# Kernel optimization log

Hardware: AMD Instinct MI355X
Metric: run time of the kernel (lower is better)

## Reference

```python
import jax, jax.numpy as jnp
import numpy as np

B, S, T, E, H, Vt, Vs, M = 16, 64, 64, 256, 512, 32000, 32000, 100
J = 2 * M + 1


def _lstm(x, lengths, Wx, Wh, b, reverse=False):
    # TF LSTMCell (forget_bias=1.0) with sequence_length masking, optional reverse_sequence.
    Bn, Tn, _ = x.shape
    Hn = Wh.shape[0]
    tpos = jnp.arange(Tn)
    ridx = None
    if reverse:
        ridx = jnp.where(tpos[None, :] < lengths[:, None], lengths[:, None] - 1 - tpos[None, :], tpos[None, :])
        x = jnp.take_along_axis(x, ridx[:, :, None], axis=1)
    mask = (tpos[:, None] < lengths[None, :])[:, :, None]  # [T,B,1]
    xT = jnp.swapaxes(x, 0, 1)  # [T,B,E]

    def step(carry, inp):
        h, c = carry
        xt, mt = inp
        g = xt @ Wx + h @ Wh + b
        i, j, f, o = jnp.split(g, 4, axis=-1)
        c_new = jax.nn.sigmoid(f + 1.0) * c + jax.nn.sigmoid(i) * jnp.tanh(j)
        h_new = jax.nn.sigmoid(o) * jnp.tanh(c_new)
        c2 = jnp.where(mt, c_new, c)
        h2 = jnp.where(mt, h_new, h)
        return (h2, c2), jnp.where(mt, h_new, jnp.zeros_like(h_new))

    init = (jnp.zeros((Bn, Hn), x.dtype), jnp.zeros((Bn, Hn), x.dtype))
    _, ys = jax.lax.scan(step, init, (xT, mask))
    ys = jnp.swapaxes(ys, 0, 1)  # [B,T,H]
    if reverse:
        ys = jnp.take_along_axis(ys, ridx[:, :, None], axis=1)
    return ys


def setup_inputs() -> dict:
    key = jax.random.key(0)
    ks = jax.random.split(key, 24)
    sc = 0.05
    n = lambda k, shape: (jax.random.normal(k, shape, jnp.float32) * sc)
    inp = {
        "sources": jax.random.randint(ks[0], (B, S), 0, Vs, jnp.int32),
        "targets": jax.random.randint(ks[1], (B, T), 0, Vt, jnp.int32),
        "targets_null": jnp.array([Vt - 1], jnp.int32),
        "target_lengths": jax.random.randint(ks[2], (B,), T // 2, T + 1, jnp.int32),
        "emb": n(ks[3], (Vt, E)),
        "nnW": n(ks[4], (E, H)),
        "nnb": jnp.zeros((H,), jnp.float32),
        "Wx_fw": n(ks[5], (E, 4 * H)),
        "Wh_fw": n(ks[6], (H, 4 * H)),
        "b_fw": jnp.zeros((4 * H,), jnp.float32),
        "Wx_bw": n(ks[7], (E, 4 * H)),
        "Wh_bw": n(ks[8], (H, 4 * H)),
        "b_bw": jnp.zeros((4 * H,), jnp.float32),
        "Wproj_e": n(ks[9], (2 * H, H)),
        "Wv": n(ks[10], (H, Vs)),
        "bv": jnp.zeros((Vs,), jnp.float32),
        "Wproj_t": n(ks[11], (2 * H, E)),
        "Wj": n(ks[12], (H, J)),
        "bj": jnp.zeros((J,), jnp.float32),
        "Wp0": n(ks[13], (H, 1)),
        "bp0": jnp.zeros((1,), jnp.float32),
    }
    return inp


def reference(sources, targets, targets_null, target_lengths, emb, nnW, nnb,
              Wx_fw, Wh_fw, b_fw, Wx_bw, Wh_bw, b_bw, Wproj_e, Wv, bv,
              Wproj_t, Wj, bj, Wp0, bp0):
    x = emb[targets]                              # [B,T,E]
    x_null = emb[targets_null]                    # [1,E]
    null_state = jnp.tanh(x_null @ nnW + nnb)     # [1,H]
    h_fw = _lstm(x, target_lengths, Wx_fw, Wh_fw, b_fw, False)
    h_bw = _lstm(x, target_lengths, Wx_bw, Wh_bw, b_bw, True)
    h_cat = jnp.concatenate([h_fw, h_bw], axis=-1)  # [B,T,2H]

    # ---- emission ----
    ts = h_cat @ Wproj_e                          # [B,T,H]
    probs = jax.nn.softmax(ts @ Wv + bv, axis=-1)             # [B,T,Vs]
    null_probs = jax.nn.softmax(null_state @ Wv + bv, axis=-1)  # [1,Vs]
    e_word = jnp.take_along_axis(probs, sources[:, None, :].astype(jnp.int32), axis=2)  # [B,T,S]
    e_null = jnp.broadcast_to(null_probs[0][sources][:, None, :], e_word.shape)
    emission = jnp.concatenate([e_word, e_null], axis=1)       # [B,2T,S]

    # ---- transition ----
    tt = jnp.tanh((h_cat @ Wproj_t) @ nnW + nnb)  # [B,T,H]
    jump = jax.nn.softmax(tt @ Wj + bj, axis=-1)  # [B,T,J]
    p0 = jax.nn.sigmoid(tt @ Wp0 + bp0)[..., 0]   # [B,T]
    Tn = targets.shape[1]
    # entry (i,j) <- jump[i, M + j - i] (the tf.map_fn gather over word_idx)
    idx = M + jnp.arange(Tn)[None, :] - jnp.arange(Tn)[:, None]  # [T,T]
    jw = jnp.take_along_axis(jump, jnp.broadcast_to(idx[None], (jump.shape[0], Tn, Tn)), axis=2)  # [B,T,T]
    eye = jnp.eye(Tn, dtype=jw.dtype)
    half = jnp.concatenate([jw, p0[:, :, None] * eye], axis=2)            # [B,T,2T]
    transition = jnp.concatenate([half, half], axis=1)                    # [B,2T,2T]
    lhalf = jnp.concatenate([jnp.log(jw), jnp.log(p0)[:, :, None] * eye], axis=2)
    transition_log = jnp.concatenate([lhalf, lhalf], axis=1)
    return emission, transition, transition_log
```

## Files before the change

kernel.cpp:

```cpp
#include <hip/hip_runtime.h>
#include <hip/hip_bf16.h>
#include <math.h>

#define Bn 16
#define Sn 64
#define Tn 64
#define En 256
#define Hn 512
#define VS 32000
#define Jn 201
#define Mn 100

#define O_HCATF  0
#define O_DENOM  524288
#define O_NULLD  525312
#define O_SLOTS  525376
#define O_HBUF   527424
#define ZERO_N   560192
#define O_NS     560192
#define O_TS     560704
#define O_TSF    1084992
#define O_TTPRE  1347136
#define O_TTPF   1609280
#define O_TT     1740352
#define O_XF     2264640
#define O_WXFW   2395712
#define O_WXBW   2657856
#define O_WPEF   2920000
#define O_WPTF   3182144
#define O_NNWF   3313216
#define O_GX     3378752
#define O_WVB    2264640

typedef __attribute__((ext_vector_type(8))) short short8;
typedef __attribute__((ext_vector_type(4))) float f32x4;

__device__ __forceinline__ float sigf(float x) { return 1.0f / (1.0f + expf(-x)); }
__device__ __forceinline__ unsigned short tobf(float x) {
    __hip_bfloat16 h = __float2bfloat16(x);
    return *reinterpret_cast<unsigned short*>(&h);
}

__device__ __forceinline__ void dconvA(const float* __restrict__ A, uint4* __restrict__ out,
                                       int K, const int* __restrict__ gidx, int g) {
    int Kd = K >> 5;
    int lane = g & 63, t = g >> 6;
    int ks = t % Kd, mt = t / Kd;
    int m = mt * 16 + (lane & 15);
    int k0 = ks * 32 + (lane >> 4) * 8;
    const float* p = (gidx ? A + (size_t)gidx[m] * K : A + (size_t)m * K) + k0;
    float4 f0 = *(const float4*)(p);
    float4 f1 = *(const float4*)(p + 4);
    unsigned short u[8] = {tobf(f0.x), tobf(f0.y), tobf(f0.z), tobf(f0.w),
                           tobf(f1.x), tobf(f1.y), tobf(f1.z), tobf(f1.w)};
    out[g] = *(uint4*)u;
}

__device__ __forceinline__ void dconvB(const float* __restrict__ B, uint4* __restrict__ out,
                                       int N, int K, int g) {
    int Kd = K >> 5;
    int lane = g & 63, t = g >> 6;
    int ks = t % Kd, nt = t / Kd;
    int n = nt * 16 + (lane & 15);
    int k0 = ks * 32 + (lane >> 4) * 8;
    const float* p = B + (size_t)k0 * N + n;
    unsigned short u[8];
#pragma unroll
    for (int j = 0; j < 8; j++) u[j] = tobf(p[(size_t)j * N]);
    out[g] = *(uint4*)u;
}

__global__ __launch_bounds__(256) void convA_k(const float* __restrict__ A,
                                               uint4* __restrict__ out, int K,
                                               const int* __restrict__ gidx) {
    dconvA(A, out, K, gidx, blockIdx.x * 256 + threadIdx.x);
}
__global__ __launch_bounds__(256) void convB_k(const float* __restrict__ B,
                                               uint4* __restrict__ out, int N, int K) {
    dconvB(B, out, N, K, blockIdx.x * 256 + threadIdx.x);
}

__global__ __launch_bounds__(256) void mega_prep_k(float4* __restrict__ zdst, int zn4,
                                                   const float* __restrict__ emb,
                                                   const int* __restrict__ targets,
                                                   uint4* __restrict__ xf,
                                                   const float* __restrict__ wxfw, uint4* __restrict__ wxfwf,
                                                   const float* __restrict__ wxbw, uint4* __restrict__ wxbwf,
                                                   const float* __restrict__ wpe, uint4* __restrict__ wpef,
                                                   const float* __restrict__ wpt, uint4* __restrict__ wptf,
                                                   const float* __restrict__ nnw, uint4* __restrict__ nnwf) {
    int blk = blockIdx.x, tid = threadIdx.x;
    if (blk < 548) {
        int i = blk * 256 + tid;
        if (i < zn4) zdst[i] = make_float4(0.f, 0.f, 0.f, 0.f);
    } else if (blk < 676) {
        dconvA(emb, xf, 256, targets, (blk - 548) * 256 + tid);
    } else if (blk < 932) {
        dconvB(wxfw, wxfwf, 2048, 256, (blk - 676) * 256 + tid);
    } else if (blk < 1188) {
        dconvB(wxbw, wxbwf, 2048, 256, (blk - 932) * 256 + tid);
    } else if (blk < 1444) {
        dconvB(wpe, wpef, 512, 1024, (blk - 1188) * 256 + tid);
    } else if (blk < 1572) {
        dconvB(wpt, wptf, 256, 1024, (blk - 1444) * 256 + tid);
    } else {
        dconvB(nnw, nnwf, 512, 256, (blk - 1572) * 256 + tid);
    }
}

template <int ACT>
__global__ __launch_bounds__(256) void gemm_mfma_k(const uint4* __restrict__ af,
                                                   const uint4* __restrict__ bf,
                                                   const float* __restrict__ bias,
                                                   float* __restrict__ C, int N, int Kd) {
    int tid = threadIdx.x, w = tid >> 6, lane = tid & 63;
    int ntb = blockIdx.x * 8 + w * 2;
    int mtb = blockIdx.y * 8;
    f32x4 acc[8][2];
#pragma unroll
    for (int i = 0; i < 8; i++)
#pragma unroll
        for (int j = 0; j < 2; j++) acc[i][j] = 0.0f;
    for (int ks = 0; ks < Kd; ++ks) {
        uint4 b0 = bf[(size_t)(ntb * Kd + ks) * 64 + lane];
        uint4 b1 = bf[(size_t)((ntb + 1) * Kd + ks) * 64 + lane];
#pragma unroll
        for (int i = 0; i < 8; i++) {
            uint4 a = af[(size_t)((mtb + i) * Kd + ks) * 64 + lane];
            acc[i][0] = __builtin_amdgcn_mfma_f32_16x16x32_bf16(
                *reinterpret_cast<short8*>(&a), *reinterpret_cast<short8*>(&b0), acc[i][0], 0, 0, 0);
            acc[i][1] = __builtin_amdgcn_mfma_f32_16x16x32_bf16(
                *reinterpret_cast<short8*>(&a), *reinterpret_cast<short8*>(&b1), acc[i][1], 0, 0, 0);
        }
    }
    int n0 = ntb * 16 + (lane & 15);
    int q = lane >> 4;
    float bs0 = bias ? bias[n0] : 0.f;
    float bs1 = bias ? bias[n0 + 16] : 0.f;
#pragma unroll
    for (int i = 0; i < 8; i++)
#pragma unroll
        for (int r = 0; r < 4; r++) {
            int m = (mtb + i) * 16 + q * 4 + r;
            float v0 = acc[i][0][r] + bs0;
            float v1 = acc[i][1][r] + bs1;
            if (ACT == 1) { v0 = tanhf(v0); v1 = tanhf(v1); }
            C[(size_t)m * N + n0] = v0;
            C[(size_t)m * N + n0 + 16] = v1;
        }
}

__global__ __launch_bounds__(256) void null_fused_k(const float* __restrict__ emb,
                                                    const int* __restrict__ tnull,
                                                    const float* __restrict__ nnW,
                                                    const float* __restrict__ nnb,
                                                    const float* __restrict__ Wv,
                                                    const float* __restrict__ bv,
                                                    float* __restrict__ ns,
                                                    float* __restrict__ nd) {
    __shared__ float xn[En];
    __shared__ float nsl[Hn];
    __shared__ float red[4];
    int t = threadIdx.x;
    xn[t] = emb[(size_t)tnull[0] * En + t];
    __syncthreads();
#pragma unroll
    for (int hh = 0; hh < 2; hh++) {
        int h = t + hh * 256;
        float a = nnb[h];
        for (int e = 0; e < En; e++) a += xn[e] * nnW[(size_t)e * Hn + h];
        float v = tanhf(a);
        nsl[h] = v;
        if (blockIdx.x == 0) ns[h] = v;
    }
    __syncthreads();
    int v = blockIdx.x * 256 + t;
    float a = bv[v];
    for (int k = 0; k < Hn; k++) a += nsl[k] * Wv[(size_t)k * VS + v];
    float e = expf(a);
    for (int o = 1; o < 64; o <<= 1) e += __shfl_xor(e, o);
    if ((t & 63) == 0) red[t >> 6] = e;
    __syncthreads();
    if (t == 0) atomicAdd(nd, red[0] + red[1] + red[2] + red[3]);
}

__global__ __launch_bounds__(256, 1) void lstm_persist_k(const float* __restrict__ wh_fw,
                                                         const float* __restrict__ wh_bw,
                                                         const float* __restrict__ gx,
                                                         const int* __restrict__ lengths,
                                                         unsigned* __restrict__ hbuf32,
                                                         unsigned* __restrict__ hcat32,
                                                         unsigned* __restrict__ slots) {
    __shared__ uint4 whf[8192];
    __shared__ float raw[32][129];
    __shared__ int lenS[16];
    int tid = threadIdx.x;
    int blk = blockIdx.x;
    int dir = blk >> 4;
    int u0 = (blk & 15) * 32;
    const float* wh = dir ? wh_bw : wh_fw;
    if (tid < 16) lenS[tid] = lengths[tid];

    for (int chunk = 0; chunk < 16; ++chunk) {
#pragma unroll
        for (int it = 0; it < 16; ++it) {
            int li = it * 256 + tid;
            int kl = li >> 7, c = li & 127;
            int g = c >> 5, ub = c & 31;
            raw[kl][c] = wh[(size_t)(chunk * 32 + kl) * 2048 + g * 512 + u0 + ub];
        }
        __syncthreads();
#pragma unroll
        for (int it = 0; it < 2; ++it) {
            int idx = tid * 2 + it;
            int w = idx >> 7, t = (idx >> 6) & 1, lane = idx & 63;
            int n = lane & 15, uu = n >> 1, p = n & 1;
            int cc = (t * 2 + p) * 32 + w * 8 + uu;
            int kb = (lane >> 4) * 8;
            unsigned short u8[8];
#pragma unroll
            for (int j = 0; j < 8; j++) u8[j] = tobf(raw[kb + j][cc]);
            whf[((w * 2 + t) * 16 + chunk) * 64 + lane] = *(uint4*)u8;
        }
        __syncthreads();
    }

    int wv = tid >> 6, lane = tid & 63;
    int n = lane & 15, uu = n >> 1, q = lane >> 4;
    int u = u0 + wv * 8 + uu;
    float creg[4] = {0.f, 0.f, 0.f, 0.f};
    unsigned short hbf[4] = {0, 0, 0, 0};

    for (int s = 0; s < 64; ++s) {
        float gxi[4], gxj[4], gxf[4], gxo[4];
#pragma unroll
        for (int r = 0; r < 4; r++) {
            int b = q * 4 + r;
            int len = lenS[b];
            int tc = dir ? (len - 1 - s) : s;
            tc = tc < 0 ? 0 : tc;
            const float* gp = gx + (size_t)dir * 2097152 + (size_t)(b * 64 + tc) * 2048 + u;
            gxi[r] = gp[0]; gxj[r] = gp[512]; gxf[r] = gp[1024]; gxo[r] = gp[1536];
        }
        const unsigned long long* hb64 =
            (const unsigned long long*)(hbuf32 + (((s & 1) * 2 + dir) * 16) * 256);
        unsigned long long h64[32];
#pragma unroll
        for (int ks = 0; ks < 16; ks++) {
            int idx = n * 128 + ks * 8 + q * 2;
            h64[2 * ks] = __hip_atomic_load(hb64 + idx, __ATOMIC_RELAXED, __HIP_MEMORY_SCOPE_AGENT);
            h64[2 * ks + 1] = __hip_atomic_load(hb64 + idx + 1, __ATOMIC_RELAXED, __HIP_MEMORY_SCOPE_AGENT);
        }
        f32x4 acc0 = {0.f, 0.f, 0.f, 0.f}, acc1 = {0.f, 0.f, 0.f, 0.f};
#pragma unroll
        for (int ks = 0; ks < 16; ks++) {
            unsigned long long av[2] = {h64[2 * ks], h64[2 * ks + 1]};
            short8 a = *reinterpret_cast<short8*>(av);
            uint4 b0 = whf[((wv * 2 + 0) * 16 + ks) * 64 + lane];
            uint4 b1 = whf[((wv * 2 + 1) * 16 + ks) * 64 + lane];
            acc0 = __builtin_amdgcn_mfma_f32_16x16x32_bf16(a, *reinterpret_cast<short8*>(&b0), acc0, 0, 0, 0);
            acc1 = __builtin_amdgcn_mfma_f32_16x16x32_bf16(a, *reinterpret_cast<short8*>(&b1), acc1, 0, 0, 0);
        }
#pragma unroll
        for (int r = 0; r < 4; r++) {
            float jvv = __shfl_xor(acc0[r], 1);
            float ovv = __shfl_xor(acc1[r], 1);
            int b = q * 4 + r;
            int len = lenS[b];
            float gi = acc0[r] + gxi[r];
            float gj = jvv + gxj[r];
            float gf = acc1[r] + gxf[r];
            float go = ovv + gxo[r];
            float cn = sigf(gf + 1.0f) * creg[r] + sigf(gi) * tanhf(gj);
            float hn = sigf(go) * tanhf(cn);
            if (s < len) { creg[r] = cn; hbf[r] = tobf(hn); }
        }
#pragma unroll
        for (int r = 0; r < 4; r++) {
            unsigned self = hbf[r];
            unsigned part = (unsigned)__shfl_xor((int)self, 2) & 0xffffu;
            if ((n & 3) == 0) {
                unsigned pk = self | (part << 16);
                int b = q * 4 + r;
                __hip_atomic_store(
                    hbuf32 + ((((s + 1) & 1) * 2 + dir) * 16 + b) * 256 + (u >> 1), pk,
                    __ATOMIC_RELAXED, __HIP_MEMORY_SCOPE_AGENT);
                int len = lenS[b];
                if (s < len) {
                    int tin = dir ? (len - 1 - s) : s;
                    int row = b * 64 + tin, col = dir * 512 + u;
                    int mt = row >> 4, ksx = col >> 5;
                    int lanep = (row & 15) | (((col >> 3) & 3) << 4);
                    hcat32[(size_t)(((mt * 32 + ksx) * 64 + lanep) * 4) + ((col & 7) >> 1)] = pk;
                }
            }
        }
        if (s == 63) break;
        __syncthreads();
        if (tid == 0)
            __hip_atomic_store(&slots[blk * 64], (unsigned)(s + 1), __ATOMIC_RELAXED,
                               __HIP_MEMORY_SCOPE_AGENT);
        if (tid < 16) {
            while (__hip_atomic_load(&slots[(dir * 16 + tid) * 64], __ATOMIC_RELAXED,
                                     __HIP_MEMORY_SCOPE_AGENT) < (unsigned)(s + 1)) {
                __builtin_amdgcn_s_sleep(1);
            }
        }
        __syncthreads();
    }
}

__global__ __launch_bounds__(256) void phaseA_mfma_k(const uint4* __restrict__ tsb,
                                                     const uint4* __restrict__ wvb,
                                                     const float* __restrict__ bv,
                                                     float* __restrict__ denom) {
    __shared__ float redL[4][128];
    int tid = threadIdx.x;
    int wave = tid >> 6, lane = tid & 63;
    int ntbase = blockIdx.x * 8 + wave * 2;
    float bv0 = bv[ntbase * 16 + (lane & 15)];
    float bv1 = bv[(ntbase + 1) * 16 + (lane & 15)];
    int q = lane >> 4;
    for (int mc = 0; mc < 8; ++mc) {
        f32x4 acc[8][2];
#pragma unroll
        for (int i = 0; i < 8; i++)
#pragma unroll
            for (int j = 0; j < 2; j++) acc[i][j] = 0.0f;
#pragma unroll 4
        for (int ks = 0; ks < 16; ++ks) {
            short8 a[8], b[2];
#pragma unroll
            for (int i = 0; i < 8; i++) {
                int mt = mc * 8 + i;
                uint4 t = tsb[(size_t)(mt * 16 + ks) * 64 + lane];
                a[i] = *reinterpret_cast<short8*>(&t);
            }
#pragma unroll
            for (int j = 0; j < 2; j++) {
                uint4 t = wvb[(size_t)((ntbase + j) * 16 + ks) * 64 + lane];
                b[j] = *reinterpret_cast<short8*>(&t);
            }
#pragma unroll
            for (int i = 0; i < 8; i++)
#pragma unroll
                for (int j = 0; j < 2; j++)
                    acc[i][j] = __builtin_amdgcn_mfma_f32_16x16x32_bf16(a[i], b[j], acc[i][j], 0, 0, 0);
        }
#pragma unroll
        for (int i = 0; i < 8; i++) {
#pragma unroll
            for (int r = 0; r < 4; r++) {
                float e = __expf(acc[i][0][r] + bv0) + __expf(acc[i][1][r] + bv1);
                e += __shfl_xor(e, 1);
                e += __shfl_xor(e, 2);
                e += __shfl_xor(e, 4);
                e += __shfl_xor(e, 8);
                if ((lane & 15) == 0) redL[wave][i * 16 + q * 4 + r] = e;
            }
        }
        __syncthreads();
        if (tid < 128) {
            float v = redL[0][tid] + redL[1][tid] + redL[2][tid] + redL[3][tid];
            atomicAdd(&denom[mc * 128 + tid], v);
        }
        __syncthreads();
    }
}

__global__ __launch_bounds__(512) void emission_k(const float* __restrict__ ts,
                                                  const float* __restrict__ Wv,
                                                  const float* __restrict__ bv,
                                                  const int* __restrict__ sources,
                                                  const float* __restrict__ ns,
                                                  const float* __restrict__ denom,
                                                  const float* __restrict__ nulld,
                                                  float* __restrict__ em) {
    __shared__ float colv[512];
    __shared__ float red[64][9];
    __shared__ float red2[8];
    __shared__ float env_s, bvc_s;
    int b = blockIdx.y, sc = blockIdx.x;
    int tid = threadIdx.x;
    for (int qq = 0; qq < 8; ++qq) {
        int s = sc * 8 + qq;
        int c = sources[b * 64 + s];
        __syncthreads();
        colv[tid] = Wv[(size_t)tid * VS + c];
        if (tid == 0) bvc_s = bv[c];
        __syncthreads();
        int r = tid & 63, ksl = tid >> 6;
        const float* tr = ts + (size_t)(b * 64 + r) * 512 + ksl * 64;
        float p = 0.f;
#pragma unroll
        for (int k4 = 0; k4 < 16; k4++) {
            float4 t4 = *(const float4*)(tr + k4 * 4);
            float4 c4 = *(const float4*)&colv[ksl * 64 + k4 * 4];
            p += t4.x * c4.x + t4.y * c4.y + t4.z * c4.z + t4.w * c4.w;
        }
        red[r][ksl] = p;
        if (tid < 8) {
            float pn = 0.f;
#pragma unroll
            for (int k4 = 0; k4 < 16; k4++) {
                float4 n4 = *(const float4*)(ns + tid * 64 + k4 * 4);
                float4 c4 = *(const float4*)&colv[tid * 64 + k4 * 4];
                pn += n4.x * c4.x + n4.y * c4.y + n4.z * c4.z + n4.w * c4.w;
            }
            red2[tid] = pn;
        }
        __syncthreads();
        if (tid < 64) {
            float dot = red[tid][0] + red[tid][1] + red[tid][2] + red[tid][3] +
                        red[tid][4] + red[tid][5] + red[tid][6] + red[tid][7];
            float ew = expf(dot + bvc_s) / denom[b * 64 + tid];
            em[(size_t)(b * 128 + tid) * 64 + s] = ew;
        } else if (tid == 64) {
            float dn = red2[0] + red2[1] + red2[2] + red2[3] +
                       red2[4] + red2[5] + red2[6] + red2[7];
            env_s = expf(dn + bvc_s) / nulld[0];
        }
        __syncthreads();
        if (tid < 64) em[(size_t)(b * 128 + 64 + tid) * 64 + s] = env_s;
    }
}

__global__ __launch_bounds__(256) void transition_k(const float* __restrict__ tt,
                                                    const float* __restrict__ Wj,
                                                    const float* __restrict__ bj,
                                                    const float* __restrict__ Wp0,
                                                    const float* __restrict__ bp0,
                                                    float* __restrict__ trans,
                                                    float* __restrict__ tlog) {
    __shared__ float ttl[512];
    __shared__ float jrow[Jn], ljrow[Jn];
    __shared__ float sred[256];
    __shared__ float p0_s, lp0_s;
    int blk = blockIdx.x;
    int b = blk >> 6, i = blk & 63;
    int tid = threadIdx.x;
    {
        const float* trr = tt + (size_t)blk * 512;
        if (tid < 128) *(float4*)&ttl[tid * 4] = *(const float4*)(trr + tid * 4);
    }
    __syncthreads();
    bool isj = tid < Jn;
    bool isp = tid == Jn;
    float l = 0.f;
    if (isj || isp) {
        const float* wb = isj ? (Wj + tid) : Wp0;
        int stride = isj ? Jn : 1;
        float a = isj ? bj[tid] : bp0[0];
        for (int k = 0; k < 512; k++) a += ttl[k] * wb[(size_t)k * stride];
        l = a;
    }
    sred[tid] = isj ? l : -1e30f;
    __syncthreads();
    for (int o = 128; o > 0; o >>= 1) {
        if (tid < o) sred[tid] = fmaxf(sred[tid], sred[tid + o]);
        __syncthreads();
    }
    float m = sred[0];
    __syncthreads();
    float ex = isj ? expf(l - m) : 0.f;
    sred[tid] = ex;
    __syncthreads();
    for (int o = 128; o > 0; o >>= 1) {
        if (tid < o) sred[tid] += sred[tid + o];
        __syncthreads();
    }
    float S = sred[0];
    if (isj) {
        jrow[tid] = ex / S;
        ljrow[tid] = (l - m) - logf(S);
    }
    if (isp) {
        float pv = 1.f / (1.f + expf(-l));
        p0_s = pv;
        lp0_s = logf(pv);
    }
    __syncthreads();
    if (tid < 128) {
        int j = tid;
        float tv, lv;
        if (j < 64) {
            int id = Mn + j - i;
            tv = jrow[id];
            lv = ljrow[id];
        } else {
            bool dg = (j - 64) == i;
            tv = dg ? p0_s : 0.f;
            lv = dg ? lp0_s : 0.f;
        }
        size_t r1 = (size_t)(b * 128 + i) * 128 + j;
        size_t r2 = (size_t)(b * 128 + 64 + i) * 128 + j;
        trans[r1] = tv;
        trans[r2] = tv;
        tlog[r1] = lv;
        tlog[r2] = lv;
    }
}

extern "C" void kernel_launch(void* const* d_in, const int* in_sizes, int n_in,
                              void* d_out, int out_size, void* d_ws, size_t ws_size,
                              hipStream_t stream) {
    const int* sources = (const int*)d_in[0];
    const int* targets = (const int*)d_in[1];
    const int* tnull = (const int*)d_in[2];
    const int* lengths = (const int*)d_in[3];
    const float* emb = (const float*)d_in[4];
    const float* nnW = (const float*)d_in[5];
    const float* nnb = (const float*)d_in[6];
    const float* Wx_fw = (const float*)d_in[7];
    const float* Wh_fw = (const float*)d_in[8];
    const float* b_fw = (const float*)d_in[9];
    const float* Wx_bw = (const float*)d_in[10];
    const float* Wh_bw = (const float*)d_in[11];
    const float* b_bw = (const float*)d_in[12];
    const float* Wproj_e = (const float*)d_in[13];
    const float* Wv = (const float*)d_in[14];
    const float* bv = (const float*)d_in[15];
    const float* Wproj_t = (const float*)d_in[16];
    const float* Wj = (const float*)d_in[17];
    const float* bj = (const float*)d_in[18];
    const float* Wp0 = (const float*)d_in[19];
    const float* bp0 = (const float*)d_in[20];

    float* ws = (float*)d_ws;
    float* out = (float*)d_out;
    float* out_em = out;
    float* out_tr = out + 131072;
    float* out_tl = out + 131072 + 262144;

    mega_prep_k<<<1636, 256, 0, stream>>>((float4*)ws, ZERO_N / 4,
                                          emb, targets, (uint4*)(ws + O_XF),
                                          Wx_fw, (uint4*)(ws + O_WXFW),
                                          Wx_bw, (uint4*)(ws + O_WXBW),
                                          Wproj_e, (uint4*)(ws + O_WPEF),
                                          Wproj_t, (uint4*)(ws + O_WPTF),
                                          nnW, (uint4*)(ws + O_NNWF));

    gemm_mfma_k<0><<<dim3(16, 8), 256, 0, stream>>>((uint4*)(ws + O_XF), (uint4*)(ws + O_WXFW),
                                                    b_fw, ws + O_GX, 2048, 8);
    gemm_mfma_k<0><<<dim3(16, 8), 256, 0, stream>>>((uint4*)(ws + O_XF), (uint4*)(ws + O_WXBW),
                                                    b_bw, ws + O_GX + 2097152, 2048, 8);

    null_fused_k<<<125, 256, 0, stream>>>(emb, tnull, nnW, nnb, Wv, bv,
                                          ws + O_NS, ws + O_NULLD);

    lstm_persist_k<<<32, 256, 0, stream>>>(Wh_fw, Wh_bw, ws + O_GX, lengths,
                                           (unsigned*)(ws + O_HBUF), (unsigned*)(ws + O_HCATF),
                                           (unsigned*)(ws + O_SLOTS));

    gemm_mfma_k<0><<<dim3(4, 8), 256, 0, stream>>>((uint4*)(ws + O_HCATF), (uint4*)(ws + O_WPEF),
                                                   nullptr, ws + O_TS, 512, 32);
    gemm_mfma_k<0><<<dim3(2, 8), 256, 0, stream>>>((uint4*)(ws + O_HCATF), (uint4*)(ws + O_WPTF),
                                                   nullptr, ws + O_TTPRE, 256, 32);
    convA_k<<<128, 256, 0, stream>>>(ws + O_TTPRE, (uint4*)(ws + O_TTPF), 256, nullptr);
    gemm_mfma_k<1><<<dim3(4, 8), 256, 0, stream>>>((uint4*)(ws + O_TTPF), (uint4*)(ws + O_NNWF),
                                                   nnb, ws + O_TT, 512, 8);
    convA_k<<<256, 256, 0, stream>>>(ws + O_TS, (uint4*)(ws + O_TSF), 512, nullptr);

    convB_k<<<8000, 256, 0, stream>>>(Wv, (uint4*)(ws + O_WVB), VS, 512);
    phaseA_mfma_k<<<250, 256, 0, stream>>>((const uint4*)(ws + O_TSF),
                                           (const uint4*)(ws + O_WVB), bv, ws + O_DENOM);

    emission_k<<<dim3(8, 16), 512, 0, stream>>>(ws + O_TS, Wv, bv, sources, ws + O_NS,
                                                ws + O_DENOM, ws + O_NULLD, out_em);

    transition_k<<<1024, 256, 0, stream>>>(ws + O_TT, Wj, bj, Wp0, bp0, out_tr, out_tl);
}
```

Baseline: 984.2 us.

## Replace LSTM slot barrier with per-step sentinel-tagged hidden-state buffers

Drops the per-timestep cross-block flag barrier in the persistent LSTM kernel. Each step now gets its own hidden-state buffer, pre-filled with a NaN bf16 sentinel by the prep kernel, and readers spin on each loaded value until the sentinel is gone. This removes two __syncthreads and the slot polling per step, so producer-to-consumer handoff becomes fine-grained. In exchange it uses more workspace (reusing the O_TS region) and depends on no real bf16 hidden value ever equalling the sentinel bit pattern and on relaxed atomics being ordered well enough.

```diff
diff --git a/kernel.cpp b/kernel.cpp
--- a/kernel.cpp
+++ b/kernel.cpp
@@ -32,6 +32,8 @@
 #define O_GX     3378752
 #define O_WVB    2264640
 
+#define HSENT 0x7FC07FC0u
+
 typedef __attribute__((ext_vector_type(8))) short short8;
 typedef __attribute__((ext_vector_type(4))) float f32x4;
 
@@ -39,6 +41,10 @@
 __device__ __forceinline__ unsigned short tobf(float x) {
     __hip_bfloat16 h = __float2bfloat16(x);
     return *reinterpret_cast<unsigned short*>(&h);
+}
+__device__ __forceinline__ bool hasSent(unsigned long long x) {
+    return ((unsigned short)(x) == 0x7FC0u) || ((unsigned short)(x >> 16) == 0x7FC0u) ||
+           ((unsigned short)(x >> 32) == 0x7FC0u) || ((unsigned short)(x >> 48) == 0x7FC0u);
 }
 
 __device__ __forceinline__ void dconvA(const float* __restrict__ A, uint4* __restrict__ out,
@@ -88,7 +94,8 @@
                                                    const float* __restrict__ wxbw, uint4* __restrict__ wxbwf,
                                                    const float* __restrict__ wpe, uint4* __restrict__ wpef,
                                                    const float* __restrict__ wpt, uint4* __restrict__ wptf,
-                                                   const float* __restrict__ nnw, uint4* __restrict__ nnwf) {
+                                                   const float* __restrict__ nnw, uint4* __restrict__ nnwf,
+                                                   uint4* __restrict__ hbuf) {
     int blk = blockIdx.x, tid = threadIdx.x;
     if (blk < 548) {
         int i = blk * 256 + tid;
@@ -103,8 +110,12 @@
         dconvB(wpe, wpef, 512, 1024, (blk - 1188) * 256 + tid);
     } else if (blk < 1572) {
         dconvB(wpt, wptf, 256, 1024, (blk - 1444) * 256 + tid);
+    } else if (blk < 1636) {
+        dconvB(nnw, nnwf, 512, 256, (blk - 1572) * 256 + tid);
     } else {
-        dconvB(nnw, nnwf, 512, 256, (blk - 1572) * 256 + tid);
+        int i = (blk - 1636) * 256 + tid;
+        unsigned v = (i < 2048) ? 0u : HSENT;
+        hbuf[i] = make_uint4(v, v, v, v);
     }
 }
 
@@ -189,8 +200,7 @@
                                                          const float* __restrict__ gx,
                                                          const int* __restrict__ lengths,
                                                          unsigned* __restrict__ hbuf32,
-                                                         unsigned* __restrict__ hcat32,
-                                                         unsigned* __restrict__ slots) {
+                                                         unsigned* __restrict__ hcat32) {
     __shared__ uint4 whf[8192];
     __shared__ float raw[32][129];
     __shared__ int lenS[16];
@@ -243,18 +253,20 @@
             gxi[r] = gp[0]; gxj[r] = gp[512]; gxf[r] = gp[1024]; gxo[r] = gp[1536];
         }
         const unsigned long long* hb64 =
-            (const unsigned long long*)(hbuf32 + (((s & 1) * 2 + dir) * 16) * 256);
-        unsigned long long h64[32];
+            (const unsigned long long*)(hbuf32 + (size_t)(s * 2 + dir) * 4096);
+        f32x4 acc0 = {0.f, 0.f, 0.f, 0.f}, acc1 = {0.f, 0.f, 0.f, 0.f};
 #pragma unroll
         for (int ks = 0; ks < 16; ks++) {
             int idx = n * 128 + ks * 8 + q * 2;
-            h64[2 * ks] = __hip_atomic_load(hb64 + idx, __ATOMIC_RELAXED, __HIP_MEMORY_SCOPE_AGENT);
-            h64[2 * ks + 1] = __hip_atomic_load(hb64 + idx + 1, __ATOMIC_RELAXED, __HIP_MEMORY_SCOPE_AGENT);
-        }
-        f32x4 acc0 = {0.f, 0.f, 0.f, 0.f}, acc1 = {0.f, 0.f, 0.f, 0.f};
-#pragma unroll
-        for (int ks = 0; ks < 16; ks++) {
-            unsigned long long av[2] = {h64[2 * ks], h64[2 * ks + 1]};
+            unsigned long long v0 =
+                __hip_atomic_load(hb64 + idx, __ATOMIC_RELAXED, __HIP_MEMORY_SCOPE_AGENT);
+            unsigned long long v1 =
+                __hip_atomic_load(hb64 + idx + 1, __ATOMIC_RELAXED, __HIP_MEMORY_SCOPE_AGENT);
+            while (hasSent(v0))
+                v0 = __hip_atomic_load(hb64 + idx, __ATOMIC_RELAXED, __HIP_MEMORY_SCOPE_AGENT);
+            while (hasSent(v1))
+                v1 = __hip_atomic_load(hb64 + idx + 1, __ATOMIC_RELAXED, __HIP_MEMORY_SCOPE_AGENT);
+            unsigned long long av[2] = {v0, v1};
             short8 a = *reinterpret_cast<short8*>(av);
             uint4 b0 = whf[((wv * 2 + 0) * 16 + ks) * 64 + lane];
             uint4 b1 = whf[((wv * 2 + 1) * 16 + ks) * 64 + lane];
@@ -282,9 +294,10 @@
             if ((n & 3) == 0) {
                 unsigned pk = self | (part << 16);
                 int b = q * 4 + r;
-                __hip_atomic_store(
-                    hbuf32 + ((((s + 1) & 1) * 2 + dir) * 16 + b) * 256 + (u >> 1), pk,
-                    __ATOMIC_RELAXED, __HIP_MEMORY_SCOPE_AGENT);
+                if (s < 63)
+                    __hip_atomic_store(
+                        hbuf32 + (size_t)((s + 1) * 2 + dir) * 4096 + b * 256 + (u >> 1), pk,
+                        __ATOMIC_RELAXED, __HIP_MEMORY_SCOPE_AGENT);
                 int len = lenS[b];
                 if (s < len) {
                     int tin = dir ? (len - 1 - s) : s;
@@ -295,18 +308,6 @@
                 }
             }
         }
-        if (s == 63) break;
-        __syncthreads();
-        if (tid == 0)
-            __hip_atomic_store(&slots[blk * 64], (unsigned)(s + 1), __ATOMIC_RELAXED,
-                               __HIP_MEMORY_SCOPE_AGENT);
-        if (tid < 16) {
-            while (__hip_atomic_load(&slots[(dir * 16 + tid) * 64], __ATOMIC_RELAXED,
-                                     __HIP_MEMORY_SCOPE_AGENT) < (unsigned)(s + 1)) {
-                __builtin_amdgcn_s_sleep(1);
-            }
-        }
-        __syncthreads();
     }
 }
 
@@ -532,13 +533,14 @@
     float* out_tr = out + 131072;
     float* out_tl = out + 131072 + 262144;
 
-    mega_prep_k<<<1636, 256, 0, stream>>>((float4*)ws, ZERO_N / 4,
+    mega_prep_k<<<2148, 256, 0, stream>>>((float4*)ws, ZERO_N / 4,
                                           emb, targets, (uint4*)(ws + O_XF),
                                           Wx_fw, (uint4*)(ws + O_WXFW),
                                           Wx_bw, (uint4*)(ws + O_WXBW),
                                           Wproj_e, (uint4*)(ws + O_WPEF),
                                           Wproj_t, (uint4*)(ws + O_WPTF),
-                                          nnW, (uint4*)(ws + O_NNWF));
+                                          nnW, (uint4*)(ws + O_NNWF),
+                                          (uint4*)(ws + O_TS));
 
     gemm_mfma_k<0><<<dim3(16, 8), 256, 0, stream>>>((uint4*)(ws + O_XF), (uint4*)(ws + O_WXFW),
                                                     b_fw, ws + O_GX, 2048, 8);
@@ -549,8 +551,7 @@
                                           ws + O_NS, ws + O_NULLD);
 
     lstm_persist_k<<<32, 256, 0, stream>>>(Wh_fw, Wh_bw, ws + O_GX, lengths,
-                                           (unsigned*)(ws + O_HBUF), (unsigned*)(ws + O_HCATF),
-                                           (unsigned*)(ws + O_SLOTS));
+                                           (unsigned*)(ws + O_TS), (unsigned*)(ws + O_HCATF));
 
     gemm_mfma_k<0><<<dim3(4, 8), 256, 0, stream>>>((uint4*)(ws + O_HCATF), (uint4*)(ws + O_WPEF),
                                                    nullptr, ws + O_TS, 512, 32);
```

Result: slower. 1.104 ms (+12.2%).

## Merge paired launches and fuse Wv bf16 conversion into phaseA via LDS

Applied to the files above, without the earlier changes.

Combines the two input-gate GEMMs, the two projection GEMMs and the two activation conversions into single launches. The null-token softmax work now runs as extra blocks of the persistent LSTM kernel, so it can overlap with the recurrence. The standalone Wv conversion pass (8000 blocks) is removed; each phaseA block converts its own Wv slice into shared memory. This saves launch overhead and a round trip of the bf16 Wv copy through global memory, at the cost of more LDS per phaseA block and of the null blocks possibly competing with the LSTM blocks for the GPU.

```diff
diff --git a/kernel.cpp b/kernel.cpp
--- a/kernel.cpp
+++ b/kernel.cpp
@@ -30,7 +30,6 @@
 #define O_WPTF   3182144
 #define O_NNWF   3313216
 #define O_GX     3378752
-#define O_WVB    2264640
 
 typedef __attribute__((ext_vector_type(8))) short short8;
 typedef __attribute__((ext_vector_type(4))) float f32x4;
@@ -70,14 +69,13 @@
     out[g] = *(uint4*)u;
 }
 
-__global__ __launch_bounds__(256) void convA_k(const float* __restrict__ A,
-                                               uint4* __restrict__ out, int K,
-                                               const int* __restrict__ gidx) {
-    dconvA(A, out, K, gidx, blockIdx.x * 256 + threadIdx.x);
-}
-__global__ __launch_bounds__(256) void convB_k(const float* __restrict__ B,
-                                               uint4* __restrict__ out, int N, int K) {
-    dconvB(B, out, N, K, blockIdx.x * 256 + threadIdx.x);
+__global__ __launch_bounds__(256) void convA2_k(const float* __restrict__ ttpre,
+                                                uint4* __restrict__ ttpf,
+                                                const float* __restrict__ ts,
+                                                uint4* __restrict__ tsf) {
+    int blk = blockIdx.x, tid = threadIdx.x;
+    if (blk < 128) dconvA(ttpre, ttpf, 256, nullptr, blk * 256 + tid);
+    else           dconvA(ts, tsf, 512, nullptr, (blk - 128) * 256 + tid);
 }
 
 __global__ __launch_bounds__(256) void mega_prep_k(float4* __restrict__ zdst, int zn4,
@@ -109,13 +107,14 @@
 }
 
 template <int ACT>
-__global__ __launch_bounds__(256) void gemm_mfma_k(const uint4* __restrict__ af,
-                                                   const uint4* __restrict__ bf,
-                                                   const float* __restrict__ bias,
-                                                   float* __restrict__ C, int N, int Kd) {
+__device__ __forceinline__ void gemm_body(const uint4* __restrict__ af,
+                                          const uint4* __restrict__ bf,
+                                          const float* __restrict__ bias,
+                                          float* __restrict__ C, int N, int Kd,
+                                          int bx, int by) {
     int tid = threadIdx.x, w = tid >> 6, lane = tid & 63;
-    int ntb = blockIdx.x * 8 + w * 2;
-    int mtb = blockIdx.y * 8;
+    int ntb = bx * 8 + w * 2;
+    int mtb = by * 8;
     f32x4 acc[8][2];
 #pragma unroll
     for (int i = 0; i < 8; i++)
@@ -150,52 +149,84 @@
         }
 }
 
-__global__ __launch_bounds__(256) void null_fused_k(const float* __restrict__ emb,
-                                                    const int* __restrict__ tnull,
-                                                    const float* __restrict__ nnW,
-                                                    const float* __restrict__ nnb,
-                                                    const float* __restrict__ Wv,
-                                                    const float* __restrict__ bv,
-                                                    float* __restrict__ ns,
-                                                    float* __restrict__ nd) {
-    __shared__ float xn[En];
-    __shared__ float nsl[Hn];
-    __shared__ float red[4];
-    int t = threadIdx.x;
-    xn[t] = emb[(size_t)tnull[0] * En + t];
-    __syncthreads();
-#pragma unroll
-    for (int hh = 0; hh < 2; hh++) {
-        int h = t + hh * 256;
-        float a = nnb[h];
-        for (int e = 0; e < En; e++) a += xn[e] * nnW[(size_t)e * Hn + h];
-        float v = tanhf(a);
-        nsl[h] = v;
-        if (blockIdx.x == 0) ns[h] = v;
-    }
-    __syncthreads();
-    int v = blockIdx.x * 256 + t;
-    float a = bv[v];
-    for (int k = 0; k < Hn; k++) a += nsl[k] * Wv[(size_t)k * VS + v];
-    float e = expf(a);
-    for (int o = 1; o < 64; o <<= 1) e += __shfl_xor(e, o);
-    if ((t & 63) == 0) red[t >> 6] = e;
-    __syncthreads();
-    if (t == 0) atomicAdd(nd, red[0] + red[1] + red[2] + red[3]);
-}
-
-__global__ __launch_bounds__(256, 1) void lstm_persist_k(const float* __restrict__ wh_fw,
-                                                         const float* __restrict__ wh_bw,
-                                                         const float* __restrict__ gx,
-                                                         const int* __restrict__ lengths,
-                                                         unsigned* __restrict__ hbuf32,
-                                                         unsigned* __restrict__ hcat32,
-                                                         unsigned* __restrict__ slots) {
+template <int ACT>
+__global__ __launch_bounds__(256) void gemm_mfma_k(const uint4* __restrict__ af,
+                                                   const uint4* __restrict__ bf,
+                                                   const float* __restrict__ bias,
+                                                   float* __restrict__ C, int N, int Kd) {
+    gemm_body<ACT>(af, bf, bias, C, N, Kd, blockIdx.x, blockIdx.y);
+}
+
+__global__ __launch_bounds__(256) void gx_gemm_k(const uint4* __restrict__ xf,
+                                                 const uint4* __restrict__ wxfwf,
+                                                 const uint4* __restrict__ wxbwf,
+                                                 const float* __restrict__ b_fw,
+                                                 const float* __restrict__ b_bw,
+                                                 float* __restrict__ gx) {
+    int bx = blockIdx.x;
+    if (bx < 16) gemm_body<0>(xf, wxfwf, b_fw, gx, 2048, 8, bx, blockIdx.y);
+    else         gemm_body<0>(xf, wxbwf, b_bw, gx + 2097152, 2048, 8, bx - 16, blockIdx.y);
+}
+
+__global__ __launch_bounds__(256) void proj_gemm_k(const uint4* __restrict__ hcatf,
+                                                   const uint4* __restrict__ wpef,
+                                                   const uint4* __restrict__ wptf,
+                                                   float* __restrict__ ts,
+                                                   float* __restrict__ ttpre) {
+    int bx = blockIdx.x;
+    if (bx < 4) gemm_body<0>(hcatf, wpef, nullptr, ts, 512, 32, bx, blockIdx.y);
+    else        gemm_body<0>(hcatf, wptf, nullptr, ttpre, 256, 32, bx - 4, blockIdx.y);
+}
+
+__global__ __launch_bounds__(256, 1) void lstm_fused_k(const float* __restrict__ wh_fw,
+                                                       const float* __restrict__ wh_bw,
+                                                       const float* __restrict__ gx,
+                                                       const int* __restrict__ lengths,
+                                                       unsigned* __restrict__ hbuf32,
+                                                       unsigned* __restrict__ hcat32,
+                                                       unsigned* __restrict__ slots,
+                                                       const float* __restrict__ Wv,
+                                                       const float* __restrict__ emb,
+                                                       const int* __restrict__ tnull,
+                                                       const float* __restrict__ nnW,
+                                                       const float* __restrict__ nnb,
+                                                       const float* __restrict__ bv,
+                                                       float* __restrict__ ns,
+                                                       float* __restrict__ nd) {
+    int blk = blockIdx.x;
+    int tid = threadIdx.x;
+
+    if (blk >= 32) {
+        __shared__ float xn[En];
+        __shared__ float nsl[Hn];
+        __shared__ float red[4];
+        int bid = blk - 32;
+        xn[tid] = emb[(size_t)tnull[0] * En + tid];
+        __syncthreads();
+#pragma unroll
+        for (int hh = 0; hh < 2; hh++) {
+            int h = tid + hh * 256;
+            float a = nnb[h];
+            for (int e = 0; e < En; e++) a += xn[e] * nnW[(size_t)e * Hn + h];
+            float v = tanhf(a);
+            nsl[h] = v;
+            if (bid == 0) ns[h] = v;
+        }
+        __syncthreads();
+        int v = bid * 256 + tid;
+        float a = bv[v];
+        for (int k = 0; k < Hn; k++) a += nsl[k] * Wv[(size_t)k * VS + v];
+        float e = expf(a);
+        for (int o = 1; o < 64; o <<= 1) e += __shfl_xor(e, o);
+        if ((tid & 63) == 0) red[tid >> 6] = e;
+        __syncthreads();
+        if (tid == 0) atomicAdd(nd, red[0] + red[1] + red[2] + red[3]);
+        return;
+    }
+
     __shared__ uint4 whf[8192];
     __shared__ float raw[32][129];
     __shared__ int lenS[16];
-    int tid = threadIdx.x;
-    int blk = blockIdx.x;
     int dir = blk >> 4;
     int u0 = (blk & 15) * 32;
     const float* wh = dir ? wh_bw : wh_fw;
@@ -311,12 +342,28 @@
 }
 
 __global__ __launch_bounds__(256) void phaseA_mfma_k(const uint4* __restrict__ tsb,
-                                                     const uint4* __restrict__ wvb,
+                                                     const float* __restrict__ Wv,
                                                      const float* __restrict__ bv,
                                                      float* __restrict__ denom) {
+    __shared__ uint4 wls[8192];
     __shared__ float redL[4][128];
     int tid = threadIdx.x;
     int wave = tid >> 6, lane = tid & 63;
+    for (int it = 0; it < 32; ++it) {
+        int g = it * 256 + tid;
+        int gl = g & 63, t = g >> 6;
+        int ks = t & 15, tl = t >> 4;
+        int nt = blockIdx.x * 8 + tl;
+        int nn = nt * 16 + (gl & 15);
+        int k0 = ks * 32 + (gl >> 4) * 8;
+        const float* p = Wv + (size_t)k0 * VS + nn;
+        unsigned short u[8];
+#pragma unroll
+        for (int j = 0; j < 8; j++) u[j] = tobf(p[(size_t)j * VS]);
+        wls[g] = *(uint4*)u;
+    }
+    __syncthreads();
+
     int ntbase = blockIdx.x * 8 + wave * 2;
     float bv0 = bv[ntbase * 16 + (lane & 15)];
     float bv1 = bv[(ntbase + 1) * 16 + (lane & 15)];
@@ -338,7 +385,7 @@
             }
 #pragma unroll
             for (int j = 0; j < 2; j++) {
-                uint4 t = wvb[(size_t)((ntbase + j) * 16 + ks) * 64 + lane];
+                uint4 t = wls[((wave * 2 + j) * 16 + ks) * 64 + lane];
                 b[j] = *reinterpret_cast<short8*>(&t);
             }
 #pragma unroll
@@ -540,30 +587,25 @@
                                           Wproj_t, (uint4*)(ws + O_WPTF),
                                           nnW, (uint4*)(ws + O_NNWF));
 
-    gemm_mfma_k<0><<<dim3(16, 8), 256, 0, stream>>>((uint4*)(ws + O_XF), (uint4*)(ws + O_WXFW),
-                                                    b_fw, ws + O_GX, 2048, 8);
-    gemm_mfma_k<0><<<dim3(16, 8), 256, 0, stream>>>((uint4*)(ws + O_XF), (uint4*)(ws + O_WXBW),
-                                                    b_bw, ws + O_GX + 2097152, 2048, 8);
-
-    null_fused_k<<<125, 256, 0, stream>>>(emb, tnull, nnW, nnb, Wv, bv,
+    gx_gemm_k<<<dim3(32, 8), 256, 0, stream>>>((uint4*)(ws + O_XF), (uint4*)(ws + O_WXFW),
+                                               (uint4*)(ws + O_WXBW), b_fw, b_bw, ws + O_GX);
+
+    lstm_fused_k<<<157, 256, 0, stream>>>(Wh_fw, Wh_bw, ws + O_GX, lengths,
+                                          (unsigned*)(ws + O_HBUF), (unsigned*)(ws + O_HCATF),
+                                          (unsigned*)(ws + O_SLOTS),
+                                          Wv, emb, tnull, nnW, nnb, bv,
                                           ws + O_NS, ws + O_NULLD);
 
-    lstm_persist_k<<<32, 256, 0, stream>>>(Wh_fw, Wh_bw, ws + O_GX, lengths,
-                                           (unsigned*)(ws + O_HBUF), (unsigned*)(ws + O_HCATF),
-                                           (unsigned*)(ws + O_SLOTS));
-
-    gemm_mfma_k<0><<<dim3(4, 8), 256, 0, stream>>>((uint4*)(ws + O_HCATF), (uint4*)(ws + O_WPEF),
-                                                   nullptr, ws + O_TS, 512, 32);
-    gemm_mfma_k<0><<<dim3(2, 8), 256, 0, stream>>>((uint4*)(ws + O_HCATF), (uint4*)(ws + O_WPTF),
-                                                   nullptr, ws + O_TTPRE, 256, 32);
-    convA_k<<<128, 256, 0, stream>>>(ws + O_TTPRE, (uint4*)(ws + O_TTPF), 256, nullptr);
+    proj_gemm_k<<<dim3(6, 8), 256, 0, stream>>>((uint4*)(ws + O_HCATF), (uint4*)(ws + O_WPEF),
+                                                (uint4*)(ws + O_WPTF), ws + O_TS, ws + O_TTPRE);
+
+    convA2_k<<<384, 256, 0, stream>>>(ws + O_TTPRE, (uint4*)(ws + O_TTPF),
+                                      ws + O_TS, (uint4*)(ws + O_TSF));
     gemm_mfma_k<1><<<dim3(4, 8), 256, 0, stream>>>((uint4*)(ws + O_TTPF), (uint4*)(ws + O_NNWF),
                                                    nnb, ws + O_TT, 512, 8);
-    convA_k<<<256, 256, 0, stream>>>(ws + O_TS, (uint4*)(ws + O_TSF), 512, nullptr);
-
-    convB_k<<<8000, 256, 0, stream>>>(Wv, (uint4*)(ws + O_WVB), VS, 512);
+
     phaseA_mfma_k<<<250, 256, 0, stream>>>((const uint4*)(ws + O_TSF),
-                                           (const uint4*)(ws + O_WVB), bv, ws + O_DENOM);
+                                           Wv, bv, ws + O_DENOM);
 
     emission_k<<<dim3(8, 16), 512, 0, stream>>>(ws + O_TS, Wv, bv, sources, ws + O_NS,
                                                 ws + O_DENOM, ws + O_NULLD, out_em);
```

Result: faster. 877.0 us (-10.9%).
